# Kernel tuning notes

Measured on AMD Instinct MI355X. Metric: run time of the kernel, lower is better.

## Reference

```python
import jax, jax.numpy as jnp
import numpy as np

N_INST, BATCH, IN_DIM, L_DIM = 256, 128, 1024, 512

def setup_inputs() -> dict:
    key = jax.random.key(0)
    k1, k2, k3, k4 = jax.random.split(key, 4)
    # glorot-uniform-ish scales
    sv = np.sqrt(6.0 / (IN_DIM + L_DIM)).astype(np.float32)
    sw = np.sqrt(6.0 / (L_DIM + 1)).astype(np.float32)
    x = jax.random.normal(k1, (N_INST, BATCH, IN_DIM), dtype=jnp.float32)
    v = jax.random.uniform(k2, (IN_DIM, L_DIM), minval=-sv, maxval=sv, dtype=jnp.float32)
    u = jax.random.uniform(k3, (IN_DIM, L_DIM), minval=-sv, maxval=sv, dtype=jnp.float32)
    w = jax.random.uniform(k4, (L_DIM, 1), minval=-sw, maxval=sw, dtype=jnp.float32)
    return {"x": x, "v": v, "u": u, "w": w}

def reference(x, v, u, w):
    # x: [n_instances, batch, in_dim]
    # Fused batched version of the per-instance loop:
    # score_i = (tanh(x_i @ v) * sigmoid(x_i @ u)) @ w, softmax over instances.
    h = jnp.tanh(jnp.einsum('nbd,dl->nbl', x, v))          # [n, b, l]
    g = jax.nn.sigmoid(jnp.einsum('nbd,dl->nbl', x, u))    # [n, b, l]
    scores = jnp.einsum('nbl,lo->nbo', h * g, w)            # [n, b, 1]
    alpha = jax.nn.softmax(scores, axis=0)                  # softmax over instance axis
    return alpha
```

## Files before the change

kernel.cpp:

```cpp
#include <hip/hip_runtime.h>
#include <stdint.h>

typedef unsigned int  u32;
typedef unsigned short u16;
typedef __bf16 v8bf __attribute__((ext_vector_type(8)));
typedef float  v4f  __attribute__((ext_vector_type(4)));

#define N_INST 256
#define BATCH  128
#define IN_DIM 1024
#define L_DIM  512
#define M_TOT  (N_INST*BATCH)
#define NSLICE 16

#define XB_BYTES   ((size_t)M_TOT * IN_DIM * 2)
#define WPK_BYTES  ((size_t)1024 * IN_DIM * 2)

__device__ inline u32 f2bf_pk(float a, float b){
  u32 ua = __builtin_bit_cast(u32, a);
  u32 ub = __builtin_bit_cast(u32, b);
  ua = (ua + 0x7FFFu + ((ua >> 16) & 1u)) >> 16;
  ub = (ub + 0x7FFFu + ((ub >> 16) & 1u)) & 0xFFFF0000u;
  return ua | ub;
}

__device__ inline void gl2lds16(const u16* g, u16* l){
  __builtin_amdgcn_global_load_lds(
      (const __attribute__((address_space(1))) u32*)(g),
      (__attribute__((address_space(3))) u32*)(l), 16, 0, 0);
}

#define PREP_XBLKS 16384
__global__ void prep(const float* __restrict__ x, const float* __restrict__ v,
                     const float* __restrict__ u, u16* __restrict__ xb,
                     u16* __restrict__ wpk){
  const int b = blockIdx.x;
  if (b < PREP_XBLKS){
    int t = b * 256 + threadIdx.x;
    int r = t >> 6, l = t & 63;
    int kk = r & 1, i = (r >> 1) & 3, h = (r >> 3) & 1, kt = (r >> 4) & 15, mb = r >> 8;
    int q = l >> 4, c = l & 15;
    int row = mb*128 + h*64 + i*16 + c;
    int k0  = kt*64 + kk*32 + q*8;
    const float* src = x + (size_t)row * IN_DIM + k0;
    float4 a0 = *reinterpret_cast<const float4*>(src);
    float4 a1 = *reinterpret_cast<const float4*>(src + 4);
    uint4 out;
    out.x = f2bf_pk(a0.x, a0.y); out.y = f2bf_pk(a0.z, a0.w);
    out.z = f2bf_pk(a1.x, a1.y); out.w = f2bf_pk(a1.z, a1.w);
    *reinterpret_cast<uint4*>(xb + (size_t)r*512 + l*8) = out;
  } else {
    int t = (b - PREP_XBLKS) * 256 + threadIdx.x;
    int r = t >> 6, l = t & 63;
    int kk = r & 1, j = (r >> 1) & 3, kt = (r >> 3) & 15, cs = r >> 7;
    int q = l >> 4, c = l & 15;
    int bcol = cs*4 + j;
    const float* src = (bcol & 1) ? u : v;
    int lcol = (bcol >> 1)*16 + c;
    int k0 = kt*64 + kk*32 + q*8;
    u32 o[4];
#pragma unroll
    for (int ii = 0; ii < 4; ++ii){
      float a  = src[(size_t)(k0 + 2*ii    ) * L_DIM + lcol];
      float bb = src[(size_t)(k0 + 2*ii + 1) * L_DIM + lcol];
      o[ii] = f2bf_pk(a, bb);
    }
    *reinterpret_cast<uint4*>(wpk + (size_t)r*512 + l*8) = make_uint4(o[0], o[1], o[2], o[3]);
  }
}


#define LOADA_K(KT, KK, B_) { const u16* ak_ = awave + (size_t)(KT)*8192 + (KK)*512;  \
  _Pragma("unroll") for (int gi_ = 0; gi_ < 4; ++gi_)                                 \
    afb[B_][gi_] = *reinterpret_cast<const v8bf*>(ak_ + gi_*1024); }

#define LOADB_ALL(BUF, KTL, KK) {                                                     \
  _Pragma("unroll") for (int j_ = 0; j_ < 4; ++j_)                                    \
    bfb[j_] = *reinterpret_cast<const v8bf*>(                                         \
      &Bs[BUF][((KTL)*8 + j_*2 + (KK))*512 + lane*8]); }

#define STEP_K(AB, DO_B, BUF, NKTL, NKK) {                                            \
  _Pragma("unroll") for (int j_ = 0; j_ < 4; ++j_){                                   \
    _Pragma("unroll") for (int gi_ = 0; gi_ < 4; ++gi_)                               \
      acc[gi_][j_] = __builtin_amdgcn_mfma_f32_16x16x32_bf16(                         \
          afb[AB][gi_], bfb[j_], acc[gi_][j_], 0, 0, 0);                              \
    if (DO_B) bfb[j_] = *reinterpret_cast<const v8bf*>(                               \
      &Bs[BUF][((NKTL)*8 + j_*2 + (NKK))*512 + lane*8]);                              \
  } }

__launch_bounds__(256, 3)
__global__ void gemm_score(const u16* __restrict__ xb, const u16* __restrict__ wpk,
                           const float* __restrict__ w, float* __restrict__ partial){
  __shared__ __align__(16) u16 Bs[2][16*512];

  const int tid  = threadIdx.x;
  const u32 bid  = blockIdx.x;
  const int xcd  = bid & 7;
  const int slot = bid >> 3;
  const int cs   = slot & 15;
  const int mr   = xcd*16 + (slot >> 4);
  const int mblk0= mr * 2;

  const int lane = tid & 63;
  const int wave = tid >> 6;
  const int q    = lane >> 4;
  const int c    = lane & 15;

  auto stageB = [&](int s, int buf){
#pragma unroll
    for (int it = 0; it < 4; ++it){
      const int rr = wave*4 + it;
      const u16* src = wpk + ((size_t)(cs*128 + s*16 + rr))*512 + lane*8;
      gl2lds16(src, &Bs[buf][rr*512 + lane*8]);
    }
  };

  const u16* awave = xb + (size_t)(mblk0 + (wave>>1))*131072
                        + (size_t)((wave&1)*4)*1024 + lane*8;

  v8bf afb[2][4];
  v8bf bfb[4];
  v4f  acc[4][4];
#pragma unroll
  for (int gi = 0; gi < 4; ++gi)
#pragma unroll
    for (int j = 0; j < 4; ++j)
      acc[gi][j] = (v4f){0.f, 0.f, 0.f, 0.f};

  stageB(0, 0);
  __syncthreads();
  LOADA_K(0, 0, 0);
  LOADB_ALL(0, 0, 0);

#pragma unroll 1
  for (int s = 0; s < 8; ++s){
    const int cur = s & 1;
    if (s < 7) stageB(s+1, cur^1);
    LOADA_K(2*s,   1, 1); STEP_K(0, 1, cur, 0, 1);
    LOADA_K(2*s+1, 0, 0); STEP_K(1, 1, cur, 1, 0);
    LOADA_K(2*s+1, 1, 1); STEP_K(0, 1, cur, 1, 1);
    if (s < 7) LOADA_K(2*s+2, 0, 0);
    STEP_K(1, 0, cur, 0, 0);
    __syncthreads();
    if (s < 7) LOADB_ALL(cur^1, 0, 0);
  }

  const float wl0 = w[cs*32 + c];
  const float wl1 = w[cs*32 + 16 + c];
  float* pout = partial + (size_t)cs * M_TOT
              + (size_t)(mblk0 + (wave>>1))*128 + (wave&1)*64;

#pragma unroll
  for (int gi = 0; gi < 4; ++gi){
#pragma unroll
    for (int r = 0; r < 4; ++r){
      float t0 = 2.f / (1.f + __expf(-2.f * acc[gi][0][r])) - 1.f;
      float s0 = 1.f / (1.f + __expf(-acc[gi][1][r]));
      float t1 = 2.f / (1.f + __expf(-2.f * acc[gi][2][r])) - 1.f;
      float s1 = 1.f / (1.f + __expf(-acc[gi][3][r]));
      float v2 = t0*s0*wl0 + t1*s1*wl1;
      v2 += __shfl_xor(v2, 1, 64);
      v2 += __shfl_xor(v2, 2, 64);
      v2 += __shfl_xor(v2, 4, 64);
      v2 += __shfl_xor(v2, 8, 64);
      if (c == 0) pout[gi*16 + q*4 + r] = v2;
    }
  }
}

__global__ void softmax_inst(const float* __restrict__ partial, float* __restrict__ out){
  __shared__ float red[N_INST];
  const int b = blockIdx.x;
  const int n = threadIdx.x;
  float s = 0.f;
#pragma unroll
  for (int i = 0; i < NSLICE; ++i) s += partial[(size_t)i * M_TOT + n*BATCH + b];
  red[n] = s; __syncthreads();
  for (int st = N_INST/2; st > 0; st >>= 1){
    if (n < st) red[n] = fmaxf(red[n], red[n + st]);
    __syncthreads();
  }
  float mx = red[0]; __syncthreads();
  float e = __expf(s - mx);
  red[n] = e; __syncthreads();
  for (int st = N_INST/2; st > 0; st >>= 1){
    if (n < st) red[n] += red[n + st];
    __syncthreads();
  }
  out[n*BATCH + b] = e / red[0];
}

extern "C" void kernel_launch(void* const* d_in, const int* in_sizes, int n_in,
                              void* d_out, int out_size, void* d_ws, size_t ws_size,
                              hipStream_t stream) {
  const float* x = (const float*)d_in[0];
  const float* v = (const float*)d_in[1];
  const float* u = (const float*)d_in[2];
  const float* w = (const float*)d_in[3];
  u16*   xb      = (u16*)d_ws;
  u16*   wpk     = (u16*)((char*)d_ws + XB_BYTES);
  float* partial = (float*)((char*)d_ws + XB_BYTES + WPK_BYTES);
  float* out     = (float*)d_out;

  prep<<<dim3(PREP_XBLKS + 512), dim3(256), 0, stream>>>(x, v, u, xb, wpk);
  gemm_score<<<dim3(2048), dim3(256), 0, stream>>>(xb, wpk, w, partial);
  softmax_inst<<<dim3(BATCH), dim3(N_INST), 0, stream>>>(partial, out);
}
```

Before: 283.2 us.

## Deepen A prefetch to full k-tiles with partial vmcnt barrier and MFMA priority

The GEMM main loop now prefetches whole 64-wide k-tiles of A into two alternating register sets, so each A load has a full k-tile of MFMA work to hide behind instead of half a tile. The per-chunk __syncthreads is replaced by an s_waitcnt vmcnt(8) plus raw s_barrier, so the eight A loads still in flight do not have to drain at the barrier. MFMA blocks are wrapped in s_setprio to favour matrix issue, and the last iteration is peeled out of the loop. The extra A register set raises VGPR pressure at 3 blocks per CU, and the hand-written vmcnt count has to match the outstanding LDS-staging loads exactly or the kernel will read incomplete data.

```diff
diff --git a/kernel.cpp b/kernel.cpp
--- a/kernel.cpp
+++ b/kernel.cpp
@@ -70,23 +70,32 @@
 }
 
 
-#define LOADA_K(KT, KK, B_) { const u16* ak_ = awave + (size_t)(KT)*8192 + (KK)*512;  \
-  _Pragma("unroll") for (int gi_ = 0; gi_ < 4; ++gi_)                                 \
-    afb[B_][gi_] = *reinterpret_cast<const v8bf*>(ak_ + gi_*1024); }
+#define LOADA_KT(KT, AF) { const u16* ak_ = awave + (size_t)(KT)*8192;                \
+  _Pragma("unroll") for (int kk_ = 0; kk_ < 2; ++kk_)                                 \
+    _Pragma("unroll") for (int gi_ = 0; gi_ < 4; ++gi_)                               \
+      AF[kk_][gi_] = *reinterpret_cast<const v8bf*>(ak_ + kk_*512 + gi_*1024); }
 
 #define LOADB_ALL(BUF, KTL, KK) {                                                     \
   _Pragma("unroll") for (int j_ = 0; j_ < 4; ++j_)                                    \
     bfb[j_] = *reinterpret_cast<const v8bf*>(                                         \
       &Bs[BUF][((KTL)*8 + j_*2 + (KK))*512 + lane*8]); }
 
-#define STEP_K(AB, DO_B, BUF, NKTL, NKK) {                                            \
+#define STEP_K2(AF, KKI, DO_B, BUF, NKTL, NKK) {                                      \
+  __builtin_amdgcn_s_setprio(1);                                                      \
   _Pragma("unroll") for (int j_ = 0; j_ < 4; ++j_){                                   \
     _Pragma("unroll") for (int gi_ = 0; gi_ < 4; ++gi_)                               \
       acc[gi_][j_] = __builtin_amdgcn_mfma_f32_16x16x32_bf16(                         \
-          afb[AB][gi_], bfb[j_], acc[gi_][j_], 0, 0, 0);                              \
+          AF[KKI][gi_], bfb[j_], acc[gi_][j_], 0, 0, 0);                              \
     if (DO_B) bfb[j_] = *reinterpret_cast<const v8bf*>(                               \
       &Bs[BUF][((NKTL)*8 + j_*2 + (NKK))*512 + lane*8]);                              \
-  } }
+  }                                                                                   \
+  __builtin_amdgcn_s_setprio(0); }
+
+#define CHUNK_BARRIER_V8 {                                                            \
+  __builtin_amdgcn_sched_barrier(0);                                                  \
+  asm volatile("s_waitcnt vmcnt(8)" ::: "memory");                                    \
+  __builtin_amdgcn_s_barrier();                                                       \
+  __builtin_amdgcn_sched_barrier(0); }
 
 __launch_bounds__(256, 3)
 __global__ void gemm_score(const u16* __restrict__ xb, const u16* __restrict__ wpk,
@@ -118,7 +127,8 @@
   const u16* awave = xb + (size_t)(mblk0 + (wave>>1))*131072
                         + (size_t)((wave&1)*4)*1024 + lane*8;
 
-  v8bf afb[2][4];
+  v8bf afA[2][4];
+  v8bf afB[2][4];
   v8bf bfb[4];
   v4f  acc[4][4];
 #pragma unroll
@@ -128,22 +138,28 @@
       acc[gi][j] = (v4f){0.f, 0.f, 0.f, 0.f};
 
   stageB(0, 0);
+  LOADA_KT(0, afA);
   __syncthreads();
-  LOADA_K(0, 0, 0);
   LOADB_ALL(0, 0, 0);
 
 #pragma unroll 1
-  for (int s = 0; s < 8; ++s){
+  for (int s = 0; s < 7; ++s){
     const int cur = s & 1;
-    if (s < 7) stageB(s+1, cur^1);
-    LOADA_K(2*s,   1, 1); STEP_K(0, 1, cur, 0, 1);
-    LOADA_K(2*s+1, 0, 0); STEP_K(1, 1, cur, 1, 0);
-    LOADA_K(2*s+1, 1, 1); STEP_K(0, 1, cur, 1, 1);
-    if (s < 7) LOADA_K(2*s+2, 0, 0);
-    STEP_K(1, 0, cur, 0, 0);
-    __syncthreads();
-    if (s < 7) LOADB_ALL(cur^1, 0, 0);
-  }
+    stageB(s+1, cur^1);
+    LOADA_KT(2*s+1, afB);
+    STEP_K2(afA, 0, 1, cur, 0, 1);
+    STEP_K2(afA, 1, 1, cur, 1, 0);
+    LOADA_KT(2*s+2, afA);
+    STEP_K2(afB, 0, 1, cur, 1, 1);
+    STEP_K2(afB, 1, 0, cur, 0, 0);
+    CHUNK_BARRIER_V8;
+    LOADB_ALL(cur^1, 0, 0);
+  }
+  LOADA_KT(15, afB);
+  STEP_K2(afA, 0, 1, 1, 0, 1);
+  STEP_K2(afA, 1, 1, 1, 1, 0);
+  STEP_K2(afB, 0, 1, 1, 1, 1);
+  STEP_K2(afB, 1, 0, 1, 0, 0);
 
   const float wl0 = w[cs*32 + c];
   const float wl1 = w[cs*32 + 16 + c];
```

Result: no change. 285.1 us (+0.7%).

## Load B fragments directly from global into registers, dropping LDS staging

Applied to the files above, without the earlier changes.

The GEMM kernel no longer stages the packed weight tiles through double-buffered shared memory with global_load_lds and block barriers. Each wave now reads both A and B fragments straight from global (L2-resident) memory into a two-deep register ping-pong, and wraps the MFMA bursts in s_setprio. This removes the LDS traffic and the __syncthreads per stage, but each of the four waves now fetches B separately, so global/L2 load traffic rises and latency hiding relies entirely on the register prefetch.

```diff
diff --git a/kernel.cpp b/kernel.cpp
--- a/kernel.cpp
+++ b/kernel.cpp
@@ -22,12 +22,6 @@
   ua = (ua + 0x7FFFu + ((ua >> 16) & 1u)) >> 16;
   ub = (ub + 0x7FFFu + ((ub >> 16) & 1u)) & 0xFFFF0000u;
   return ua | ub;
-}
-
-__device__ inline void gl2lds16(const u16* g, u16* l){
-  __builtin_amdgcn_global_load_lds(
-      (const __attribute__((address_space(1))) u32*)(g),
-      (__attribute__((address_space(3))) u32*)(l), 16, 0, 0);
 }
 
 #define PREP_XBLKS 16384
@@ -70,29 +64,29 @@
 }
 
 
-#define LOADA_K(KT, KK, B_) { const u16* ak_ = awave + (size_t)(KT)*8192 + (KK)*512;  \
+#define LOADA2(KT, KK, P) { const u16* ak_ = awave + (size_t)(KT)*8192 + (KK)*512;    \
   _Pragma("unroll") for (int gi_ = 0; gi_ < 4; ++gi_)                                 \
-    afb[B_][gi_] = *reinterpret_cast<const v8bf*>(ak_ + gi_*1024); }
+    af2[P][gi_] = *reinterpret_cast<const v8bf*>(ak_ + gi_*1024); }
 
-#define LOADB_ALL(BUF, KTL, KK) {                                                     \
+#define LOADB2(KT, KK, P) { const u16* bk_ = bwave + (size_t)((KT)*8 + (KK))*512;     \
   _Pragma("unroll") for (int j_ = 0; j_ < 4; ++j_)                                    \
-    bfb[j_] = *reinterpret_cast<const v8bf*>(                                         \
-      &Bs[BUF][((KTL)*8 + j_*2 + (KK))*512 + lane*8]); }
+    bf2[P][j_] = *reinterpret_cast<const v8bf*>(bk_ + j_*1024); }
 
-#define STEP_K(AB, DO_B, BUF, NKTL, NKK) {                                            \
+#define STEP_S(P, DO_R, NKT, NKK) {                                                   \
+  __builtin_amdgcn_s_setprio(1);                                                      \
   _Pragma("unroll") for (int j_ = 0; j_ < 4; ++j_){                                   \
     _Pragma("unroll") for (int gi_ = 0; gi_ < 4; ++gi_)                               \
       acc[gi_][j_] = __builtin_amdgcn_mfma_f32_16x16x32_bf16(                         \
-          afb[AB][gi_], bfb[j_], acc[gi_][j_], 0, 0, 0);                              \
-    if (DO_B) bfb[j_] = *reinterpret_cast<const v8bf*>(                               \
-      &Bs[BUF][((NKTL)*8 + j_*2 + (NKK))*512 + lane*8]);                              \
-  } }
+          af2[P][gi_], bf2[P][j_], acc[gi_][j_], 0, 0, 0);                            \
+    if (DO_R) bf2[P][j_] = *reinterpret_cast<const v8bf*>(                            \
+        bwave + (size_t)((NKT)*8 + j_*2 + (NKK))*512);                                \
+  }                                                                                   \
+  __builtin_amdgcn_s_setprio(0);                                                      \
+  if (DO_R) LOADA2(NKT, NKK, P); }
 
 __launch_bounds__(256, 3)
 __global__ void gemm_score(const u16* __restrict__ xb, const u16* __restrict__ wpk,
                            const float* __restrict__ w, float* __restrict__ partial){
-  __shared__ __align__(16) u16 Bs[2][16*512];
-
   const int tid  = threadIdx.x;
   const u32 bid  = blockIdx.x;
   const int xcd  = bid & 7;
@@ -106,20 +100,12 @@
   const int q    = lane >> 4;
   const int c    = lane & 15;
 
-  auto stageB = [&](int s, int buf){
-#pragma unroll
-    for (int it = 0; it < 4; ++it){
-      const int rr = wave*4 + it;
-      const u16* src = wpk + ((size_t)(cs*128 + s*16 + rr))*512 + lane*8;
-      gl2lds16(src, &Bs[buf][rr*512 + lane*8]);
-    }
-  };
-
   const u16* awave = xb + (size_t)(mblk0 + (wave>>1))*131072
                         + (size_t)((wave&1)*4)*1024 + lane*8;
+  const u16* bwave = wpk + (size_t)cs*128*512 + lane*8;
 
-  v8bf afb[2][4];
-  v8bf bfb[4];
+  v8bf af2[2][4];
+  v8bf bf2[2][4];
   v4f  acc[4][4];
 #pragma unroll
   for (int gi = 0; gi < 4; ++gi)
@@ -127,23 +113,16 @@
     for (int j = 0; j < 4; ++j)
       acc[gi][j] = (v4f){0.f, 0.f, 0.f, 0.f};
 
-  stageB(0, 0);
-  __syncthreads();
-  LOADA_K(0, 0, 0);
-  LOADB_ALL(0, 0, 0);
+  LOADB2(0, 0, 0); LOADA2(0, 0, 0);
+  LOADB2(0, 1, 1); LOADA2(0, 1, 1);
 
 #pragma unroll 1
-  for (int s = 0; s < 8; ++s){
-    const int cur = s & 1;
-    if (s < 7) stageB(s+1, cur^1);
-    LOADA_K(2*s,   1, 1); STEP_K(0, 1, cur, 0, 1);
-    LOADA_K(2*s+1, 0, 0); STEP_K(1, 1, cur, 1, 0);
-    LOADA_K(2*s+1, 1, 1); STEP_K(0, 1, cur, 1, 1);
-    if (s < 7) LOADA_K(2*s+2, 0, 0);
-    STEP_K(1, 0, cur, 0, 0);
-    __syncthreads();
-    if (s < 7) LOADB_ALL(cur^1, 0, 0);
+  for (int kt = 0; kt < 15; ++kt){
+    STEP_S(0, 1, kt+1, 0);
+    STEP_S(1, 1, kt+1, 1);
   }
+  STEP_S(0, 0, 0, 0);
+  STEP_S(1, 0, 0, 0);
 
   const float wl0 = w[cs*32 + c];
   const float wl1 = w[cs*32 + 16 + c];
```

After: 290.7 us. 2.7% more time.
